# Optimization experiments

Measured on AMD Instinct MI355X. Metric: run time of the kernel, lower is better.

## Reference

```python
import jax, jax.numpy as jnp
import numpy as np

S = 0.1          # slab half-width: |sum(y)| <= S
R2 = 0.02        # ball radius squared: ||y||^2 <= R2
EPS = 1e-12


def _project(z):
    """Euclidean projection of each row of z onto {y : |1^T y|<=S, ||y||^2<=R2}.

    KKT case analysis:
      1) project onto slab only; accept if inside ball
      2) project onto ball only; accept if inside slab
      3) both constraints active: y = c*z + ((sign(t)*S - c*t)/n)*1 with
         c = sqrt((n*R2 - S^2) / (n*||z||^2 - t^2)),  t = 1^T z.
    """
    n = z.shape[-1]
    t = jnp.sum(z, axis=-1, keepdims=True)                       # [B,1]
    zz = jnp.sum(z * z, axis=-1, keepdims=True)                  # [B,1]

    # case 1: slab projection (contains z itself when already feasible)
    y1 = z + (jnp.clip(t, -S, S) - t) / n
    ok1 = jnp.sum(y1 * y1, axis=-1, keepdims=True) <= R2

    # case 2: ball projection
    znorm = jnp.sqrt(jnp.maximum(zz, EPS))
    scale = jnp.minimum(1.0, jnp.sqrt(R2) / znorm)
    y2 = z * scale
    ok2 = jnp.abs(t) * scale <= S

    # case 3: both active
    denom = jnp.maximum(n * zz - t * t, EPS)                     # >= 0 by Cauchy-Schwarz
    c = jnp.sqrt(jnp.maximum(n * R2 - S * S, 0.0) / denom)
    sp = jnp.sign(t) * S
    y3 = c * z + (sp - c * t) / n

    return jnp.where(ok1, y1, jnp.where(ok2, y2, y3))


def setup_inputs() -> dict:
    key = jax.random.key(0)
    k1, k2, k3 = jax.random.split(key, 3)
    B, D_in, D_out = 65536, 512, 256
    x = jax.random.normal(k1, (B, D_in), dtype=jnp.float32)
    # params (scaled so z = W@x - b straddles the feasible region boundary)
    W = 0.01 * jax.random.normal(k2, (D_out, D_in), dtype=jnp.float32)
    b = 0.01 * jax.random.normal(k3, (D_out,), dtype=jnp.float32)
    return {"x": x, "W": W, "b": b}


def reference(x, W, b):
    z = x @ W.T - b                                              # [B, D_out]
    return _project(z)
```

## Files before the change

### kernel.cpp

```cpp
#include <hip/hip_runtime.h>


typedef __bf16 bf16x8 __attribute__((ext_vector_type(8)));
typedef float f32x4 __attribute__((ext_vector_type(4)));

#define BM 32
#define BN 256
#define BK 64
#define THREADS 256
#define APITCH 144

__device__ __forceinline__ unsigned short f2bf(float f) {
    unsigned u = __builtin_bit_cast(unsigned, f);
    u += 0x7fffu + ((u >> 16) & 1u);
    return (unsigned short)(u >> 16);
}

__global__ void wconv_kernel(const float* __restrict__ W,
                             unsigned short* __restrict__ Wb) {
    int i = (blockIdx.x * 256 + threadIdx.x) * 4;
    float4 v = *(const float4*)(W + i);
    ushort4 h;
    h.x = f2bf(v.x); h.y = f2bf(v.y); h.z = f2bf(v.z); h.w = f2bf(v.w);
    *(ushort4*)(Wb + i) = h;
}

__global__ __launch_bounds__(THREADS, 4)
void proj_gemm_kernel(const float* __restrict__ x,
                      const unsigned short* __restrict__ Wb,
                      const float* __restrict__ b,
                      float* __restrict__ out) {
    __shared__ alignas(16) unsigned short Bbuf[BN * BK];
    __shared__ alignas(16) unsigned char  Abuf[BM * APITCH];

    const int tid  = threadIdx.x;
    const int lane = tid & 63;
    const int wn   = tid >> 6;
    const int ln   = lane & 15;
    const int quad = lane >> 4;
    const int m0   = blockIdx.x * BM;

    const int arow = tid >> 3;
    const int kq   = tid & 7;
    const float* xbase = x + (long)(m0 + arow) * 512 + kq * 4;

    const int b_r0 = wn * 64 + (lane >> 3);
    const int b_cg = (lane & 7) ^ (lane >> 3);

    f32x4 acc[2][4];
    #pragma unroll
    for (int mi = 0; mi < 2; ++mi)
        #pragma unroll
        for (int ni = 0; ni < 4; ++ni)
            acc[mi][ni] = (f32x4){0.f, 0.f, 0.f, 0.f};

    for (int kt = 0; kt < 8; ++kt) {
        const int k0 = kt * BK;
        __syncthreads();
        #pragma unroll
        for (int j = 0; j < 8; ++j) {
            const unsigned short* src =
                Wb + (long)(b_r0 + j * 8) * 512 + k0 + b_cg * 8;
            __builtin_amdgcn_global_load_lds(
                (const __attribute__((address_space(1))) void*)src,
                (__attribute__((address_space(3))) void*)(unsigned long)(unsigned int)
                    (unsigned long)(uintptr_t)&Bbuf[(wn * 8 + j) * 512],
                16, 0, 0);
        }
        {
            float4 v0 = *(const float4*)(xbase + k0);
            float4 v1 = *(const float4*)(xbase + k0 + 32);
            ushort4 h0, h1;
            h0.x = f2bf(v0.x); h0.y = f2bf(v0.y); h0.z = f2bf(v0.z); h0.w = f2bf(v0.w);
            h1.x = f2bf(v1.x); h1.y = f2bf(v1.y); h1.z = f2bf(v1.z); h1.w = f2bf(v1.w);
            *(ushort4*)(Abuf + arow * APITCH + kq * 8)      = h0;
            *(ushort4*)(Abuf + arow * APITCH + kq * 8 + 64) = h1;
        }
        __syncthreads();

        #pragma unroll
        for (int ks = 0; ks < 2; ++ks) {
            bf16x8 bf[4];
            #pragma unroll
            for (int ni = 0; ni < 4; ++ni) {
                const int r  = wn * 64 + ni * 16 + ln;
                const int cc = (ks * 4 + quad) ^ (ln & 7);
                bf[ni] = *(const bf16x8*)&Bbuf[r * 64 + cc * 8];
            }
            #pragma unroll
            for (int mi = 0; mi < 2; ++mi) {
                const int row = mi * 16 + ln;
                bf16x8 af = *(const bf16x8*)
                    (Abuf + row * APITCH + ks * 64 + quad * 16);
                #pragma unroll
                for (int ni = 0; ni < 4; ++ni)
                    acc[mi][ni] = __builtin_amdgcn_mfma_f32_16x16x32_bf16(
                        af, bf[ni], acc[mi][ni], 0, 0, 0);
            }
        }
    }

    float bb[4];
    #pragma unroll
    for (int ni = 0; ni < 4; ++ni) bb[ni] = b[wn * 64 + ni * 16 + ln];
    #pragma unroll
    for (int mi = 0; mi < 2; ++mi)
        #pragma unroll
        for (int ni = 0; ni < 4; ++ni)
            #pragma unroll
            for (int r = 0; r < 4; ++r)
                acc[mi][ni][r] -= bb[ni];

    __syncthreads();
    float* P  = (float*)Abuf;
    float* AB = P + 32 * 8;

    #pragma unroll
    for (int mi = 0; mi < 2; ++mi) {
        #pragma unroll
        for (int r = 0; r < 4; ++r) {
            float s1 = 0.f, s2 = 0.f;
            #pragma unroll
            for (int ni = 0; ni < 4; ++ni) {
                float v = acc[mi][ni][r];
                s1 += v; s2 += v * v;
            }
            #pragma unroll
            for (int off = 1; off < 16; off <<= 1) {
                s1 += __shfl_xor(s1, off, 64);
                s2 += __shfl_xor(s2, off, 64);
            }
            if (ln == 0) {
                int row = mi * 16 + quad * 4 + r;
                P[row * 8 + wn * 2 + 0] = s1;
                P[row * 8 + wn * 2 + 1] = s2;
            }
        }
    }
    __syncthreads();

    if (tid < 32) {
        int row = tid;
        float t  = P[row*8+0] + P[row*8+2] + P[row*8+4] + P[row*8+6];
        float zz = P[row*8+1] + P[row*8+3] + P[row*8+5] + P[row*8+7];
        const float S = 0.1f, R2 = 0.02f, nf = 256.f, inv_n = 1.f / 256.f;
        float tc    = fminf(fmaxf(t, -S), S);
        float beta1 = (tc - t) * inv_n;
        float ny1   = zz + 2.f * beta1 * t + nf * beta1 * beta1;
        float alpha, beta;
        if (ny1 <= R2) {
            alpha = 1.f; beta = beta1;
        } else {
            float znorm = sqrtf(fmaxf(zz, 1e-12f));
            float scale = fminf(1.f, 0.14142135623730951f / znorm);
            if (fabsf(t) * scale <= S) {
                alpha = scale; beta = 0.f;
            } else {
                float denom = fmaxf(nf * zz - t * t, 1e-12f);
                float c  = sqrtf(5.11f / denom);
                float sp = (t > 0.f) ? S : ((t < 0.f) ? -S : 0.f);
                alpha = c; beta = (sp - c * t) * inv_n;
            }
        }
        AB[row*2+0] = alpha;
        AB[row*2+1] = beta;
    }
    __syncthreads();

    #pragma unroll
    for (int mi = 0; mi < 2; ++mi) {
        #pragma unroll
        for (int r = 0; r < 4; ++r) {
            int row = mi * 16 + quad * 4 + r;
            float alpha = AB[row*2+0];
            float beta  = AB[row*2+1];
            float* orow = out + (long)(m0 + row) * 256 + wn * 64 + ln;
            #pragma unroll
            for (int ni = 0; ni < 4; ++ni)
                orow[ni*16] = alpha * acc[mi][ni][r] + beta;
        }
    }
}

extern "C" void kernel_launch(void* const* d_in, const int* in_sizes, int n_in,
                              void* d_out, int out_size, void* d_ws, size_t ws_size,
                              hipStream_t stream) {
    const float* x = (const float*)d_in[0];
    const float* W = (const float*)d_in[1];
    const float* b = (const float*)d_in[2];
    float* out = (float*)d_out;
    unsigned short* Wb = (unsigned short*)d_ws;

    const int Dout = in_sizes[2];
    const int Din  = in_sizes[1] / Dout;
    const int Btot = in_sizes[0] / Din;

    wconv_kernel<<<(Dout * Din) / (256 * 4), 256, 0, stream>>>(W, Wb);
    proj_gemm_kernel<<<Btot / BM, THREADS, 0, stream>>>(x, Wb, b, out);
}
```

Before: 228.6 us.

## Double row tile to 64 with 8 waves sharing each W tile, swizzle A smem

Each block now covers 64 rows with 512 threads arranged as 2x4 waves, so every bf16 W tile staged in LDS is reused by twice as many rows and W reload traffic per output row is halved. The A tile switches from a padded pitch to an XOR-swizzled 128-byte row layout, with each thread converting 8 contiguous floats and writing them as one 16-byte store. Launch bounds ask for 8 waves/SIMD-level occupancy at the larger block size, which may squeeze registers. The block count halves, which may reduce latency hiding across the device.

```diff
diff --git a/kernel.cpp b/kernel.cpp
--- a/kernel.cpp
+++ b/kernel.cpp
@@ -3,12 +3,12 @@
 
 typedef __bf16 bf16x8 __attribute__((ext_vector_type(8)));
 typedef float f32x4 __attribute__((ext_vector_type(4)));
-
-#define BM 32
+typedef unsigned short ushort8 __attribute__((ext_vector_type(8)));
+
+#define BM 64
 #define BN 256
 #define BK 64
-#define THREADS 256
-#define APITCH 144
+#define THREADS 512
 
 __device__ __forceinline__ unsigned short f2bf(float f) {
     unsigned u = __builtin_bit_cast(unsigned, f);
@@ -25,26 +25,29 @@
     *(ushort4*)(Wb + i) = h;
 }
 
-__global__ __launch_bounds__(THREADS, 4)
+__global__ __launch_bounds__(THREADS, 8)
 void proj_gemm_kernel(const float* __restrict__ x,
                       const unsigned short* __restrict__ Wb,
                       const float* __restrict__ b,
                       float* __restrict__ out) {
     __shared__ alignas(16) unsigned short Bbuf[BN * BK];
-    __shared__ alignas(16) unsigned char  Abuf[BM * APITCH];
+    __shared__ alignas(16) unsigned short Abuf[BM * BK];
 
     const int tid  = threadIdx.x;
     const int lane = tid & 63;
-    const int wn   = tid >> 6;
+    const int wv   = tid >> 6;
+    const int wm   = wv >> 2;
+    const int wn   = wv & 3;
     const int ln   = lane & 15;
     const int quad = lane >> 4;
     const int m0   = blockIdx.x * BM;
 
     const int arow = tid >> 3;
     const int kq   = tid & 7;
-    const float* xbase = x + (long)(m0 + arow) * 512 + kq * 4;
-
-    const int b_r0 = wn * 64 + (lane >> 3);
+    const float* xbase = x + (long)(m0 + arow) * 512 + kq * 8;
+    const unsigned awb = (unsigned)((arow * 128 + kq * 16) ^ ((arow & 7) << 4));
+
+    const int b_r0 = wv * 32 + (lane >> 3);
     const int b_cg = (lane & 7) ^ (lane >> 3);
 
     f32x4 acc[2][4];
@@ -58,23 +61,22 @@
         const int k0 = kt * BK;
         __syncthreads();
         #pragma unroll
-        for (int j = 0; j < 8; ++j) {
+        for (int j = 0; j < 4; ++j) {
             const unsigned short* src =
                 Wb + (long)(b_r0 + j * 8) * 512 + k0 + b_cg * 8;
             __builtin_amdgcn_global_load_lds(
                 (const __attribute__((address_space(1))) void*)src,
                 (__attribute__((address_space(3))) void*)(unsigned long)(unsigned int)
-                    (unsigned long)(uintptr_t)&Bbuf[(wn * 8 + j) * 512],
+                    (unsigned long)(uintptr_t)&Bbuf[(wv * 4 + j) * 512],
                 16, 0, 0);
         }
         {
             float4 v0 = *(const float4*)(xbase + k0);
-            float4 v1 = *(const float4*)(xbase + k0 + 32);
-            ushort4 h0, h1;
-            h0.x = f2bf(v0.x); h0.y = f2bf(v0.y); h0.z = f2bf(v0.z); h0.w = f2bf(v0.w);
-            h1.x = f2bf(v1.x); h1.y = f2bf(v1.y); h1.z = f2bf(v1.z); h1.w = f2bf(v1.w);
-            *(ushort4*)(Abuf + arow * APITCH + kq * 8)      = h0;
-            *(ushort4*)(Abuf + arow * APITCH + kq * 8 + 64) = h1;
+            float4 v1 = *(const float4*)(xbase + k0 + 4);
+            ushort8 h;
+            h[0] = f2bf(v0.x); h[1] = f2bf(v0.y); h[2] = f2bf(v0.z); h[3] = f2bf(v0.w);
+            h[4] = f2bf(v1.x); h[5] = f2bf(v1.y); h[6] = f2bf(v1.z); h[7] = f2bf(v1.w);
+            *(ushort8*)((char*)Abuf + awb) = h;
         }
         __syncthreads();
 
@@ -89,9 +91,10 @@
             }
             #pragma unroll
             for (int mi = 0; mi < 2; ++mi) {
-                const int row = mi * 16 + ln;
-                bf16x8 af = *(const bf16x8*)
-                    (Abuf + row * APITCH + ks * 64 + quad * 16);
+                const int row = wm * 32 + mi * 16 + ln;
+                const unsigned arb =
+                    (unsigned)(row * 128 + ((((ks << 2) | quad) ^ (ln & 7)) << 4));
+                bf16x8 af = *(const bf16x8*)((const char*)Abuf + arb);
                 #pragma unroll
                 for (int ni = 0; ni < 4; ++ni)
                     acc[mi][ni] = __builtin_amdgcn_mfma_f32_16x16x32_bf16(
@@ -113,7 +116,7 @@
 
     __syncthreads();
     float* P  = (float*)Abuf;
-    float* AB = P + 32 * 8;
+    float* AB = P + 64 * 8;
 
     #pragma unroll
     for (int mi = 0; mi < 2; ++mi) {
@@ -131,7 +134,7 @@
                 s2 += __shfl_xor(s2, off, 64);
             }
             if (ln == 0) {
-                int row = mi * 16 + quad * 4 + r;
+                int row = wm * 32 + mi * 16 + quad * 4 + r;
                 P[row * 8 + wn * 2 + 0] = s1;
                 P[row * 8 + wn * 2 + 1] = s2;
             }
@@ -139,7 +142,7 @@
     }
     __syncthreads();
 
-    if (tid < 32) {
+    if (tid < 64) {
         int row = tid;
         float t  = P[row*8+0] + P[row*8+2] + P[row*8+4] + P[row*8+6];
         float zz = P[row*8+1] + P[row*8+3] + P[row*8+5] + P[row*8+7];
@@ -171,7 +174,7 @@
     for (int mi = 0; mi < 2; ++mi) {
         #pragma unroll
         for (int r = 0; r < 4; ++r) {
-            int row = mi * 16 + quad * 4 + r;
+            int row = wm * 32 + mi * 16 + quad * 4 + r;
             float alpha = AB[row*2+0];
             float beta  = AB[row*2+1];
             float* orow = out + (long)(m0 + row) * 256 + wn * 64 + ln;
```

Measured after the change: 247.1 us. +8.1%, slower.
